# Performance work log

Hardware: AMD Instinct MI355X
Metric: run time of the kernel (lower is better)

Reference implementation:

```python
import jax, jax.numpy as jnp
import numpy as np

B, T, N, D = 16, 12, 325, 1
K, H = 3, 64
ST, Z, LH = 95, 32, 128
MI = ST + Z  # 127


def _mlp(x, w1, b1, w2, b2):
    return jnp.maximum(x @ w1 + b1, 0.0) @ w2 + b2


def setup_inputs() -> dict:
    key = jax.random.key(0)
    ks = jax.random.split(key, 20)
    inp = {
        "G": jax.random.normal(ks[0], (K, N, N), jnp.float32) * (1.0 / np.sqrt(N)),
        "x": jax.random.normal(ks[1], (B, T, N, D), jnp.float32),
        "meta_input": jax.random.normal(ks[2], (B, N, MI), jnp.float32),
    }
    s = 0.02
    outs = {"lwg": K * (D + H) * 2 * H, "lbg": 2 * H, "lwu": K * (D + H) * H, "lbu": H}
    i = 3
    for name, od in outs.items():
        inp[name + "_w1"] = jax.random.normal(ks[i], (MI, LH), jnp.float32) * s; i += 1
        inp[name + "_b1"] = jnp.zeros((LH,), jnp.float32)
        inp[name + "_w2"] = jax.random.normal(ks[i], (LH, od), jnp.float32) * s; i += 1
        inp[name + "_b2"] = jnp.zeros((od,), jnp.float32)
    return inp


def reference(G, x, meta_input,
              lwg_w1, lwg_b1, lwg_w2, lwg_b2,
              lbg_w1, lbg_b1, lbg_w2, lbg_b2,
              lwu_w1, lwu_b1, lwu_w2, lwu_b2,
              lbu_w1, lbu_b1, lbu_w2, lbu_b2):
    # hypernetwork: per-(batch, node) GCN weights
    Wg = _mlp(meta_input, lwg_w1, lwg_b1, lwg_w2, lwg_b2).reshape(B, N, K * (D + H), 2 * H)
    bg = _mlp(meta_input, lbg_w1, lbg_b1, lbg_w2, lbg_b2)          # [B,N,2H]
    Wu = _mlp(meta_input, lwu_w1, lwu_b1, lwu_w2, lwu_b2).reshape(B, N, K * (D + H), H)
    bu = _mlp(meta_input, lbu_w1, lbu_b1, lbu_w2, lbu_b2)          # [B,N,H]

    def gcn(inp, W, b):
        # Chebyshev hops stacked along k (matches torch.cat over k-blocks)
        sup = jnp.einsum('knm,bmi->bnki', G, inp)                  # [B,N,K,i]
        sup = sup.reshape(B, N, -1)                                # [B,N,K*i]
        return jnp.einsum('bni,bnih->bnh', sup, W) + b

    def step(h, xt):
        comb = jnp.concatenate([xt, h], axis=-1)                   # [B,N,D+H]
        zr = jax.nn.sigmoid(gcn(comb, Wg, bg))
        z, r = zr[..., :H], zr[..., H:]
        cand = jnp.concatenate([xt, r * h], axis=-1)
        n = jnp.tanh(gcn(cand, Wu, bu))
        h = z * n + (1.0 - z) * h
        return h, h

    h0 = jnp.zeros((B, N, H), x.dtype)
    h_last, hs = jax.lax.scan(step, h0, jnp.moveaxis(x, 1, 0))     # hs: [T,B,N,H]
    return jnp.moveaxis(hs, 0, 1), h_last
```

## Files before the change

kernel.cpp:

```cpp
#include <hip/hip_runtime.h>
#include <hip/hip_bf16.h>
#include <stdint.h>

#define Bc   16
#define Tc   12
#define Nc   325
#define Kc   3
#define Hc   64
#define MIc  127
#define LHc  128
#define BNc  (Bc*Nc)
#define SUPW 195
#define NCg  (SUPW*2*Hc)
#define NCu  (SUPW*Hc)
#define NT4  82
#define MP   163

typedef _Float16 half8  __attribute__((ext_vector_type(8)));
typedef _Float16 half2v __attribute__((ext_vector_type(2)));
typedef float    f32x4  __attribute__((ext_vector_type(4)));

static __device__ __forceinline__ float bflo(unsigned int u) {
    return __uint_as_float(u << 16);
}
static __device__ __forceinline__ float bfhi(unsigned int u) {
    return __uint_as_float(u & 0xffff0000u);
}
static __device__ __forceinline__ unsigned short f2bf(float f) {
    unsigned int u = __float_as_uint(f);
    unsigned int r = (u + 0x7fffu + ((u >> 16) & 1u)) >> 16;
    return (unsigned short)r;
}
static __device__ __forceinline__ float fdot2f(half2v a, half2v b, float c) {
#if defined(__has_builtin)
#if __has_builtin(__builtin_amdgcn_fdot2)
    return __builtin_amdgcn_fdot2(a, b, c, false);
#else
    return c + (float)a[0] * (float)b[0] + (float)a[1] * (float)b[1];
#endif
#else
    return c + (float)a[0] * (float)b[0] + (float)a[1] * (float)b[1];
#endif
}
static __device__ __forceinline__ unsigned int packh2(float a, float b) {
    half2v h; h[0] = (_Float16)a; h[1] = (_Float16)b;
    return *(unsigned int*)&h;
}

__global__ __launch_bounds__(128) void meta1_kernel(
    const float* __restrict__ meta,
    const float* __restrict__ w1a, const float* __restrict__ b1a,
    const float* __restrict__ w1b, const float* __restrict__ b1b,
    const float* __restrict__ w1c, const float* __restrict__ b1c,
    const float* __restrict__ w1d, const float* __restrict__ b1d,
    _Float16* __restrict__ r1a, _Float16* __restrict__ r1b,
    _Float16* __restrict__ r1c, _Float16* __restrict__ r1d)
{
    __shared__ float mrow[4][128];
    const int bn0 = blockIdx.x * 4;
    const int l   = threadIdx.x;
#pragma unroll
    for (int r = 0; r < 4; r++)
        mrow[r][l] = (l < MIc) ? meta[(size_t)(bn0 + r) * MIc + l] : 0.f;
    __syncthreads();

    const float* w1s[4] = {w1a, w1b, w1c, w1d};
    const float* b1s[4] = {b1a, b1b, b1c, b1d};
    _Float16*    os[4]  = {r1a, r1b, r1c, r1d};
#pragma unroll
    for (int s = 0; s < 4; s++) {
        const float* w = w1s[s];
        float acc[4];
        const float bv = b1s[s][l];
#pragma unroll
        for (int r = 0; r < 4; r++) acc[r] = bv;
        for (int m = 0; m < MIc; m++) {
            float wv = w[m * LHc + l];
#pragma unroll
            for (int r = 0; r < 4; r++) acc[r] = fmaf(mrow[r][m], wv, acc[r]);
        }
#pragma unroll
        for (int r = 0; r < 4; r++)
            os[s][(size_t)(bn0 + r) * LHc + l] = (_Float16)fmaxf(acc[r], 0.f);
    }
}

__global__ __launch_bounds__(256) void transpose_w2_kernel(
    const float* __restrict__ w2, _Float16* __restrict__ w2t, int NC)
{
    __shared__ float Ls[128][65];
    const int c0 = blockIdx.x * 64;
    const int t  = threadIdx.x;
    {
        const int c  = t & 63;
        const int kb = t >> 6;
        for (int k = kb; k < 128; k += 4) {
            int cc = c0 + c;
            Ls[k][c] = (cc < NC) ? w2[(size_t)k * NC + cc] : 0.f;
        }
    }
    __syncthreads();
    {
        const int k  = t & 127;
        const int ch = t >> 7;
        for (int c = ch; c < 64; c += 2) {
            int cc = c0 + c;
            if (cc < NC) w2t[(size_t)cc * 128 + k] = (_Float16)Ls[k][c];
        }
    }
}

template<bool BF16OUT>
__global__ __launch_bounds__(256) void meta2_mfma_kernel(
    const _Float16* __restrict__ A,
    const _Float16* __restrict__ Bt,
    const float* __restrict__ bias,
    void* __restrict__ outp, int NC, int nrows)
{
    __shared__ __align__(16) _Float16 As[64][136];
    __shared__ __align__(16) _Float16 Bs[64][136];
    __shared__ unsigned short Cs[64][72];
    const int t  = threadIdx.x;
    const int w  = t >> 6;
    const int l  = t & 63;
    const int r0 = blockIdx.x * 64;
    const int c0 = blockIdx.y * 64;

#pragma unroll
    for (int p = 0; p < 4; p++) {
        const int gid = p * 256 + t;
        const int row = gid >> 4;
        const int cg  = gid & 15;
        half8 av = (half8)(_Float16)0.f;
        if (r0 + row < nrows) av = *(const half8*)(A + (size_t)(r0 + row) * 128 + cg * 8);
        *(half8*)&As[row][cg * 8] = av;
        half8 bv = *(const half8*)(Bt + (size_t)(c0 + row) * 128 + cg * 8);
        *(half8*)&Bs[row][cg * 8] = bv;
    }
    __syncthreads();

    const int lr = l & 15;
    const int lk = l >> 4;

    half8 aF[4];
#pragma unroll
    for (int kk = 0; kk < 4; kk++)
        aF[kk] = *(const half8*)&As[w * 16 + lr][kk * 32 + lk * 8];

    f32x4 acc[4];
#pragma unroll
    for (int j = 0; j < 4; j++) acc[j] = (f32x4)0.f;

#pragma unroll
    for (int j = 0; j < 4; j++)
#pragma unroll
        for (int kk = 0; kk < 4; kk++) {
            half8 bF = *(const half8*)&Bs[j * 16 + lr][kk * 32 + lk * 8];
            acc[j] = __builtin_amdgcn_mfma_f32_16x16x32_f16(aF[kk], bF, acc[j], 0, 0, 0);
        }

    if (BF16OUT) {
#pragma unroll
        for (int j = 0; j < 4; j++) {
            const float bv = bias[c0 + j * 16 + lr];
#pragma unroll
            for (int q = 0; q < 4; q++)
                Cs[w * 16 + lk * 4 + q][j * 16 + lr] = f2bf(acc[j][q] + bv);
        }
        __syncthreads();
        const int rl  = t >> 2;
        const int cp  = t & 3;
        const int row = r0 + rl;
        if (row < nrows) {
            const uint4* src = (const uint4*)&Cs[rl][cp * 16];
            uint4* dst = (uint4*)((unsigned short*)outp + (size_t)row * NC + c0 + cp * 16);
            dst[0] = src[0];
            dst[1] = src[1];
        }
    } else {
#pragma unroll
        for (int j = 0; j < 4; j++) {
            const int col = c0 + j * 16 + lr;
            const float bv = bias[col];
#pragma unroll
            for (int q = 0; q < 4; q++) {
                const int row = r0 + w * 16 + lk * 4 + q;
                if (row < nrows)
                    ((float*)outp)[(size_t)row * NC + col] = acc[j][q] + bv;
            }
        }
    }
}

__global__ __launch_bounds__(256) void gx_kernel(
    const float* __restrict__ G, const float* __restrict__ x,
    float* __restrict__ GX)
{
    __shared__ __align__(16) float Gs[32][36];
    __shared__ __align__(16) float Xs[32][65];
    const int k   = blockIdx.x;
    const int n0  = blockIdx.y * 32;
    const int tb0 = blockIdx.z * 64;
    const int t   = threadIdx.x;
    const int j   = t & 63;
    const int ng  = t >> 6;

    float acc[8] = {0.f,0.f,0.f,0.f,0.f,0.f,0.f,0.f};

    for (int mc = 0; mc < 11; mc++) {
        const int m0 = mc * 32;
        __syncthreads();
        {
            const int ln  = t >> 3;
            const int lm0 = (t & 7) * 4;
            const int gn  = n0 + ln;
#pragma unroll
            for (int u = 0; u < 4; u++) {
                int m = m0 + lm0 + u;
                Gs[lm0 + u][ln] = (gn < Nc && m < Nc) ? G[((size_t)k * Nc + gn) * Nc + m] : 0.f;
            }
        }
        {
            const int row = t >> 2;
            const int ms  = (t & 3) * 8;
            const float* xr = x + (size_t)(tb0 + row) * Nc;
#pragma unroll
            for (int u = 0; u < 8; u++) {
                int m = m0 + ms + u;
                Xs[ms + u][row] = (m < Nc) ? xr[m] : 0.f;
            }
        }
        __syncthreads();
#pragma unroll
        for (int mm = 0; mm < 32; mm++) {
            float xv = Xs[mm][j];
            float4 ga = *(const float4*)&Gs[mm][ng * 8];
            float4 gb = *(const float4*)&Gs[mm][ng * 8 + 4];
            acc[0] = fmaf(ga.x, xv, acc[0]);
            acc[1] = fmaf(ga.y, xv, acc[1]);
            acc[2] = fmaf(ga.z, xv, acc[2]);
            acc[3] = fmaf(ga.w, xv, acc[3]);
            acc[4] = fmaf(gb.x, xv, acc[4]);
            acc[5] = fmaf(gb.y, xv, acc[5]);
            acc[6] = fmaf(gb.z, xv, acc[6]);
            acc[7] = fmaf(gb.w, xv, acc[7]);
        }
    }

    const int tb = tb0 + j;
    const int b  = tb / Tc;
    const int tv = tb % Tc;
    float* gxp = GX + (((size_t)tv * Bc + b) * Kc + k) * Nc;
#pragma unroll
    for (int i = 0; i < 8; i++) {
        int n = n0 + ng * 8 + i;
        if (n < Nc) gxp[n] = acc[i];
    }
}

__global__ __launch_bounds__(256) void fused_gates_kernel(
    const float* __restrict__ G, const float* __restrict__ hbuf,
    const float* __restrict__ GX, const unsigned short* __restrict__ Wg,
    const float* __restrict__ bg, float* __restrict__ zbuf,
    float* __restrict__ rhbuf, int tt, int bStart)
{
    __shared__ unsigned int Ht2[MP][64];
    __shared__ unsigned int Gt2[12][MP+1];
    __shared__ float supL[4][200];
    const int bx = blockIdx.x;
    const int bl = bx / NT4;
    const int n0 = (bx % NT4) * 4;
    const int b  = bStart + bl;
    const int t  = threadIdx.x;
    const int j  = t & 63;
    const int ng = t >> 6;

    {
        const float* hb = hbuf + (size_t)b * Nc * Hc;
        for (int mp = ng; mp < MP; mp += 4) {
            const int m0 = 2 * mp;
            float h0 = hb[(size_t)m0 * Hc + j];
            float h1 = (m0 + 1 < Nc) ? hb[(size_t)(m0 + 1) * Hc + j] : 0.f;
            Ht2[mp][j] = packh2(h0, h1);
        }
    }
#pragma unroll
    for (int r = 0; r < 12; r++) {
        const int nn = r / 3, k = r % 3;
        int n = n0 + nn; if (n >= Nc) n = Nc - 1;
        const float* gr = G + ((size_t)k * Nc + n) * Nc;
        for (int mp = t; mp < MP; mp += 256) {
            const int m0 = 2 * mp;
            float g0 = gr[m0];
            float g1 = (m0 + 1 < Nc) ? gr[m0 + 1] : 0.f;
            Gt2[r][mp] = packh2(g0, g1);
        }
    }
    __syncthreads();

    float a0 = 0.f, a1 = 0.f, a2v = 0.f;
    const unsigned int* g0p = &Gt2[ng * 3 + 0][0];
    const unsigned int* g1p = &Gt2[ng * 3 + 1][0];
    const unsigned int* g2p = &Gt2[ng * 3 + 2][0];
#pragma unroll 2
    for (int mp = 0; mp < MP; mp++) {
        unsigned int hu = Ht2[mp][j];
        half2v hh = *(half2v*)&hu;
        unsigned int u0 = g0p[mp], u1 = g1p[mp], u2 = g2p[mp];
        a0  = fdot2f(*(half2v*)&u0, hh, a0);
        a1  = fdot2f(*(half2v*)&u1, hh, a1);
        a2v = fdot2f(*(half2v*)&u2, hh, a2v);
    }
    supL[ng][0 * 65 + 1 + j] = a0;
    supL[ng][1 * 65 + 1 + j] = a1;
    supL[ng][2 * 65 + 1 + j] = a2v;
    if (t < 12) {
        const int nn = t / 3, k = t - (t / 3) * 3;
        const int n = n0 + nn;
        supL[nn][k * 65] = (n < Nc) ?
            GX[(((size_t)tt * Bc + b) * Kc + k) * Nc + n] : 0.f;
    }
    __syncthreads();

    const int n = n0 + ng;
    if (n >= Nc) return;
    const int lane = t & 63;
    const int c = lane & 15;
    const int g = lane >> 4;
    const size_t bnL = (size_t)bl * Nc + n;
    const size_t bng = (size_t)b  * Nc + n;
    const unsigned short* wrow = Wg + bnL * NCg;
    float a2[8] = {0.f,0.f,0.f,0.f,0.f,0.f,0.f,0.f};

    for (int i0 = 0; i0 < SUPW; i0 += 16) {
#pragma unroll
        for (int uu = 0; uu < 4; uu++) {
            const int i = i0 + uu * 4 + g;
            if (i < SUPW) {
                uint4 v = *(const uint4*)(wrow + (size_t)i * 128 + c * 8);
                float s = supL[ng][i];
                a2[0] = fmaf(s, bflo(v.x), a2[0]);
                a2[1] = fmaf(s, bfhi(v.x), a2[1]);
                a2[2] = fmaf(s, bflo(v.y), a2[2]);
                a2[3] = fmaf(s, bfhi(v.y), a2[3]);
                a2[4] = fmaf(s, bflo(v.z), a2[4]);
                a2[5] = fmaf(s, bfhi(v.z), a2[5]);
                a2[6] = fmaf(s, bflo(v.w), a2[6]);
                a2[7] = fmaf(s, bfhi(v.w), a2[7]);
            }
        }
    }
#pragma unroll
    for (int w8 = 0; w8 < 8; w8++) {
        a2[w8] += __shfl_xor(a2[w8], 16, 64);
        a2[w8] += __shfl_xor(a2[w8], 32, 64);
    }
    if (g == 0) {
#pragma unroll
        for (int w8 = 0; w8 < 8; w8++) {
            const int h2 = c * 8 + w8;
            const float pre = a2[w8] + bg[bng * (2 * Hc) + h2];
            const float zr  = 1.f / (1.f + expf(-pre));
            if (h2 < Hc) zbuf[bng * Hc + h2] = zr;
            else {
                const int hh = h2 - Hc;
                rhbuf[bng * Hc + hh] = zr * hbuf[bng * Hc + hh];
            }
        }
    }
}

__global__ __launch_bounds__(256) void fused_update_kernel(
    const float* __restrict__ G, const float* __restrict__ rhbuf,
    const float* __restrict__ GX, const unsigned short* __restrict__ Wu,
    const float* __restrict__ bu, const float* __restrict__ zbuf,
    float* __restrict__ hbuf, float* __restrict__ outp, int tt, int bStart)
{
    __shared__ unsigned int Ht2[MP][64];
    __shared__ unsigned int Gt2[12][MP+1];
    __shared__ float supL[4][200];
    const int bx = blockIdx.x;
    const int bl = bx / NT4;
    const int n0 = (bx % NT4) * 4;
    const int b  = bStart + bl;
    const int t  = threadIdx.x;
    const int j  = t & 63;
    const int ng = t >> 6;

    {
        const float* hb = rhbuf + (size_t)b * Nc * Hc;
        for (int mp = ng; mp < MP; mp += 4) {
            const int m0 = 2 * mp;
            float h0 = hb[(size_t)m0 * Hc + j];
            float h1 = (m0 + 1 < Nc) ? hb[(size_t)(m0 + 1) * Hc + j] : 0.f;
            Ht2[mp][j] = packh2(h0, h1);
        }
    }
#pragma unroll
    for (int r = 0; r < 12; r++) {
        const int nn = r / 3, k = r % 3;
        int n = n0 + nn; if (n >= Nc) n = Nc - 1;
        const float* gr = G + ((size_t)k * Nc + n) * Nc;
        for (int mp = t; mp < MP; mp += 256) {
            const int m0 = 2 * mp;
            float g0 = gr[m0];
            float g1 = (m0 + 1 < Nc) ? gr[m0 + 1] : 0.f;
            Gt2[r][mp] = packh2(g0, g1);
        }
    }
    __syncthreads();

    float a0 = 0.f, a1 = 0.f, a2v = 0.f;
    const unsigned int* g0p = &Gt2[ng * 3 + 0][0];
    const unsigned int* g1p = &Gt2[ng * 3 + 1][0];
    const unsigned int* g2p = &Gt2[ng * 3 + 2][0];
#pragma unroll 2
    for (int mp = 0; mp < MP; mp++) {
        unsigned int hu = Ht2[mp][j];
        half2v hh = *(half2v*)&hu;
        unsigned int u0 = g0p[mp], u1 = g1p[mp], u2 = g2p[mp];
        a0  = fdot2f(*(half2v*)&u0, hh, a0);
        a1  = fdot2f(*(half2v*)&u1, hh, a1);
        a2v = fdot2f(*(half2v*)&u2, hh, a2v);
    }
    supL[ng][0 * 65 + 1 + j] = a0;
    supL[ng][1 * 65 + 1 + j] = a1;
    supL[ng][2 * 65 + 1 + j] = a2v;
    if (t < 12) {
        const int nn = t / 3, k = t - (t / 3) * 3;
        const int n = n0 + nn;
        supL[nn][k * 65] = (n < Nc) ?
            GX[(((size_t)tt * Bc + b) * Kc + k) * Nc + n] : 0.f;
    }
    __syncthreads();

    const int n = n0 + ng;
    if (n >= Nc) return;
    const int lane = t & 63;
    const int c = lane & 7;
    const int g = lane >> 3;
    const size_t bnL = (size_t)bl * Nc + n;
    const size_t bng = (size_t)b  * Nc + n;
    const unsigned short* wrow = Wu + bnL * NCu;
    float a2[8] = {0.f,0.f,0.f,0.f,0.f,0.f,0.f,0.f};

    for (int i0 = 0; i0 < SUPW; i0 += 32) {
#pragma unroll
        for (int uu = 0; uu < 4; uu++) {
            const int i = i0 + uu * 8 + g;
            if (i < SUPW) {
                uint4 v = *(const uint4*)(wrow + (size_t)i * 64 + c * 8);
                float s = supL[ng][i];
                a2[0] = fmaf(s, bflo(v.x), a2[0]);
                a2[1] = fmaf(s, bfhi(v.x), a2[1]);
                a2[2] = fmaf(s, bflo(v.y), a2[2]);
                a2[3] = fmaf(s, bfhi(v.y), a2[3]);
                a2[4] = fmaf(s, bflo(v.z), a2[4]);
                a2[5] = fmaf(s, bfhi(v.z), a2[5]);
                a2[6] = fmaf(s, bflo(v.w), a2[6]);
                a2[7] = fmaf(s, bfhi(v.w), a2[7]);
            }
        }
    }
#pragma unroll
    for (int w8 = 0; w8 < 8; w8++) {
        a2[w8] += __shfl_xor(a2[w8], 8, 64);
        a2[w8] += __shfl_xor(a2[w8], 16, 64);
        a2[w8] += __shfl_xor(a2[w8], 32, 64);
    }
    if (g == 0) {
#pragma unroll
        for (int w8 = 0; w8 < 8; w8++) {
            const int hh = c * 8 + w8;
            const float npre = a2[w8] + bu[bng * Hc + hh];
            const float nn_t = tanhf(npre);
            const float z    = zbuf[bng * Hc + hh];
            const float hold = hbuf[bng * Hc + hh];
            const float hnew = fmaf(z, nn_t - hold, hold);
            hbuf[bng * Hc + hh] = hnew;
            outp[(((size_t)b * Tc + tt) * Nc + n) * Hc + hh] = hnew;
            if (tt == Tc - 1)
                outp[(size_t)Bc * Tc * Nc * Hc + bng * Hc + hh] = hnew;
        }
    }
}

extern "C" void kernel_launch(void* const* d_in, const int* in_sizes, int n_in,
                              void* d_out, int out_size, void* d_ws, size_t ws_size,
                              hipStream_t stream)
{
    const float* G        = (const float*)d_in[0];
    const float* x        = (const float*)d_in[1];
    const float* meta     = (const float*)d_in[2];
    const float* lwg_w1   = (const float*)d_in[3];
    const float* lwg_b1   = (const float*)d_in[4];
    const float* lwg_w2   = (const float*)d_in[5];
    const float* lwg_b2   = (const float*)d_in[6];
    const float* lbg_w1   = (const float*)d_in[7];
    const float* lbg_b1   = (const float*)d_in[8];
    const float* lbg_w2   = (const float*)d_in[9];
    const float* lbg_b2   = (const float*)d_in[10];
    const float* lwu_w1   = (const float*)d_in[11];
    const float* lwu_b1   = (const float*)d_in[12];
    const float* lwu_w2   = (const float*)d_in[13];
    const float* lwu_b2   = (const float*)d_in[14];
    const float* lbu_w1   = (const float*)d_in[15];
    const float* lbu_b1   = (const float*)d_in[16];
    const float* lbu_w2   = (const float*)d_in[17];
    const float* lbu_b2   = (const float*)d_in[18];

    auto alignup = [](size_t b) { return (b + 255) & ~(size_t)255; };
    const size_t miscBytes =
        alignup((size_t)BNc * 2 * Hc * 4) +
        alignup((size_t)BNc * Hc * 4) +
        4 * alignup((size_t)BNc * LHc * 2) +
        alignup((size_t)NCg * 128 * 2) +
        alignup((size_t)NCu * 128 * 2) +
        alignup((size_t)128 * 128 * 2) +
        alignup((size_t)64 * 128 * 2) +
        alignup((size_t)Tc * Bc * Kc * Nc * 4) +
        3 * alignup((size_t)BNc * Hc * 4);

    int Bch = 0;
    const int cand[4] = {8, 4, 2, 1};
    for (int ci = 0; ci < 4; ci++) {
        size_t BNch = (size_t)cand[ci] * Nc;
        size_t need = miscBytes + alignup(BNch * NCg * 2) + alignup(BNch * NCu * 2);
        if (need <= ws_size) { Bch = cand[ci]; break; }
    }
    if (Bch == 0) return;
    const int nChunks = Bc / Bch;
    const int BNch    = Bch * Nc;

    char* ws = (char*)d_ws;
    size_t off = 0;
    auto alloc = [&](size_t bytes) -> char* {
        char* p = ws + off;
        off += (bytes + 255) & ~(size_t)255;
        return p;
    };
    unsigned short* Wg = (unsigned short*)alloc((size_t)BNch * NCg * 2);
    unsigned short* Wu = (unsigned short*)alloc((size_t)BNch * NCu * 2);
    float* bgbuf  = (float*)alloc((size_t)BNc * 2 * Hc * 4);
    float* bubuf  = (float*)alloc((size_t)BNc * Hc * 4);
    _Float16* r1g  = (_Float16*)alloc((size_t)BNc * LHc * 2);
    _Float16* r1bg = (_Float16*)alloc((size_t)BNc * LHc * 2);
    _Float16* r1u  = (_Float16*)alloc((size_t)BNc * LHc * 2);
    _Float16* r1bu = (_Float16*)alloc((size_t)BNc * LHc * 2);
    _Float16* w2tg  = (_Float16*)alloc((size_t)NCg * 128 * 2);
    _Float16* w2tu  = (_Float16*)alloc((size_t)NCu * 128 * 2);
    _Float16* w2tbg = (_Float16*)alloc((size_t)128 * 128 * 2);
    _Float16* w2tbu = (_Float16*)alloc((size_t)64 * 128 * 2);
    float* GX    = (float*)alloc((size_t)Tc * Bc * Kc * Nc * 4);
    float* hbuf  = (float*)alloc((size_t)BNc * Hc * 4);
    float* zbuf  = (float*)alloc((size_t)BNc * Hc * 4);
    float* rhbuf = (float*)alloc((size_t)BNc * Hc * 4);
    if (off > ws_size) return;

    float* out = (float*)d_out;

    hipMemsetAsync(hbuf, 0, (size_t)BNc * Hc * 4, stream);

    meta1_kernel<<<BNc / 4, 128, 0, stream>>>(
        meta, lwg_w1, lwg_b1, lbg_w1, lbg_b1, lwu_w1, lwu_b1, lbu_w1, lbu_b1,
        r1g, r1bg, r1u, r1bu);

    transpose_w2_kernel<<<(NCg + 63) / 64, 256, 0, stream>>>(lwg_w2, w2tg, NCg);
    transpose_w2_kernel<<<(NCu + 63) / 64, 256, 0, stream>>>(lwu_w2, w2tu, NCu);
    transpose_w2_kernel<<<2, 256, 0, stream>>>(lbg_w2, w2tbg, 2 * Hc);
    transpose_w2_kernel<<<1, 256, 0, stream>>>(lbu_w2, w2tbu, Hc);

    meta2_mfma_kernel<false><<<dim3((BNc + 63) / 64, (2 * Hc) / 64), 256, 0, stream>>>(
        r1bg, w2tbg, lbg_b2, (void*)bgbuf, 2 * Hc, BNc);
    meta2_mfma_kernel<false><<<dim3((BNc + 63) / 64, Hc / 64), 256, 0, stream>>>(
        r1bu, w2tbu, lbu_b2, (void*)bubuf, Hc, BNc);

    gx_kernel<<<dim3(Kc, 11, 3), 256, 0, stream>>>(G, x, GX);

    for (int ch = 0; ch < nChunks; ch++) {
        const int bStart  = ch * Bch;
        const int bnStart = bStart * Nc;

        meta2_mfma_kernel<true><<<dim3((BNch + 63) / 64, NCg / 64), 256, 0, stream>>>(
            r1g + (size_t)bnStart * LHc, w2tg, lwg_b2, (void*)Wg, NCg, BNch);
        meta2_mfma_kernel<true><<<dim3((BNch + 63) / 64, NCu / 64), 256, 0, stream>>>(
            r1u + (size_t)bnStart * LHc, w2tu, lwu_b2, (void*)Wu, NCu, BNch);

        for (int tt = 0; tt < Tc; tt++) {
            fused_gates_kernel<<<Bch * NT4, 256, 0, stream>>>(
                G, hbuf, GX, Wg, bgbuf, zbuf, rhbuf, tt, bStart);
            fused_update_kernel<<<Bch * NT4, 256, 0, stream>>>(
                G, rhbuf, GX, Wu, bubuf, zbuf, hbuf, out, tt, bStart);
        }
    }
}
```

Before: 2.369 ms.

## Assign one node per block and chunk graph-diffusion staging through small LDS tiles

Fused gate and update kernels now process a single node per block, staging the hidden state and G rows in 32-pair chunks rather than whole-matrix LDS buffers. The weight GEMV is split across all four waves, with partial sums reduced through shared memory. LDS use shrinks sharply and the launch bound requests six blocks per CU to raise occupancy. In exchange, each block re-reads and repacks the full hidden state for only one node, which quadruples that traffic and adds per-chunk barriers.

```diff
diff --git a/kernel.cpp b/kernel.cpp
--- a/kernel.cpp
+++ b/kernel.cpp
@@ -13,8 +13,8 @@
 #define SUPW 195
 #define NCg  (SUPW*2*Hc)
 #define NCu  (SUPW*Hc)
-#define NT4  82
 #define MP   163
+#define MCH  6
 
 typedef _Float16 half8  __attribute__((ext_vector_type(8)));
 typedef _Float16 half2v __attribute__((ext_vector_type(2)));
@@ -258,108 +258,104 @@
     }
 }
 
-__global__ __launch_bounds__(256) void fused_gates_kernel(
+__global__ __launch_bounds__(256, 6) void fused_gates_kernel(
     const float* __restrict__ G, const float* __restrict__ hbuf,
     const float* __restrict__ GX, const unsigned short* __restrict__ Wg,
     const float* __restrict__ bg, float* __restrict__ zbuf,
     float* __restrict__ rhbuf, int tt, int bStart)
 {
-    __shared__ unsigned int Ht2[MP][64];
-    __shared__ unsigned int Gt2[12][MP+1];
-    __shared__ float supL[4][200];
+    __shared__ unsigned int Hc2[32][64];
+    __shared__ unsigned int Gc2[3][34];
+    __shared__ float supL[208];
+    __shared__ float pS[4][16][8];
     const int bx = blockIdx.x;
-    const int bl = bx / NT4;
-    const int n0 = (bx % NT4) * 4;
+    const int bl = bx / Nc;
+    const int n  = bx % Nc;
     const int b  = bStart + bl;
     const int t  = threadIdx.x;
-    const int j  = t & 63;
-    const int ng = t >> 6;
-
-    {
-        const float* hb = hbuf + (size_t)b * Nc * Hc;
-        for (int mp = ng; mp < MP; mp += 4) {
-            const int m0 = 2 * mp;
-            float h0 = hb[(size_t)m0 * Hc + j];
-            float h1 = (m0 + 1 < Nc) ? hb[(size_t)(m0 + 1) * Hc + j] : 0.f;
-            Ht2[mp][j] = packh2(h0, h1);
-        }
-    }
-#pragma unroll
-    for (int r = 0; r < 12; r++) {
-        const int nn = r / 3, k = r % 3;
-        int n = n0 + nn; if (n >= Nc) n = Nc - 1;
-        const float* gr = G + ((size_t)k * Nc + n) * Nc;
-        for (int mp = t; mp < MP; mp += 256) {
-            const int m0 = 2 * mp;
-            float g0 = gr[m0];
+    const int lane = t & 63;
+    const int w  = t >> 6;
+    const int j  = lane;
+
+    const float* hb = hbuf + (size_t)b * Nc * Hc;
+    float accA = 0.f;
+
+    for (int c6 = 0; c6 < MCH; c6++) {
+        const int mpB = c6 * 32;
+        __syncthreads();
+#pragma unroll
+        for (int p = 0; p < 8; p++) {
+            const int idx = p * 256 + t;
+            const int mpl = idx >> 6;
+            const int jj  = idx & 63;
+            const int m0  = 2 * (mpB + mpl);
+            float h0 = (m0 < Nc)     ? hb[(size_t)m0 * Hc + jj]       : 0.f;
+            float h1 = (m0 + 1 < Nc) ? hb[(size_t)(m0 + 1) * Hc + jj] : 0.f;
+            Hc2[mpl][jj] = packh2(h0, h1);
+        }
+        if (t < 96) {
+            const int kk  = t >> 5;
+            const int mpl = t & 31;
+            const int m0  = 2 * (mpB + mpl);
+            const float* gr = G + ((size_t)kk * Nc + n) * Nc;
+            float g0 = (m0 < Nc)     ? gr[m0]     : 0.f;
             float g1 = (m0 + 1 < Nc) ? gr[m0 + 1] : 0.f;
-            Gt2[r][mp] = packh2(g0, g1);
-        }
-    }
-    __syncthreads();
-
-    float a0 = 0.f, a1 = 0.f, a2v = 0.f;
-    const unsigned int* g0p = &Gt2[ng * 3 + 0][0];
-    const unsigned int* g1p = &Gt2[ng * 3 + 1][0];
-    const unsigned int* g2p = &Gt2[ng * 3 + 2][0];
-#pragma unroll 2
-    for (int mp = 0; mp < MP; mp++) {
-        unsigned int hu = Ht2[mp][j];
-        half2v hh = *(half2v*)&hu;
-        unsigned int u0 = g0p[mp], u1 = g1p[mp], u2 = g2p[mp];
-        a0  = fdot2f(*(half2v*)&u0, hh, a0);
-        a1  = fdot2f(*(half2v*)&u1, hh, a1);
-        a2v = fdot2f(*(half2v*)&u2, hh, a2v);
-    }
-    supL[ng][0 * 65 + 1 + j] = a0;
-    supL[ng][1 * 65 + 1 + j] = a1;
-    supL[ng][2 * 65 + 1 + j] = a2v;
-    if (t < 12) {
-        const int nn = t / 3, k = t - (t / 3) * 3;
-        const int n = n0 + nn;
-        supL[nn][k * 65] = (n < Nc) ?
-            GX[(((size_t)tt * Bc + b) * Kc + k) * Nc + n] : 0.f;
-    }
-    __syncthreads();
-
-    const int n = n0 + ng;
-    if (n >= Nc) return;
-    const int lane = t & 63;
+            Gc2[kk][mpl] = packh2(g0, g1);
+        }
+        __syncthreads();
+        if (w < 3) {
+            const unsigned int* gp = &Gc2[w][0];
+#pragma unroll
+            for (int mpl = 0; mpl < 32; mpl++) {
+                unsigned int hu = Hc2[mpl][j];
+                unsigned int gu = gp[mpl];
+                accA = fdot2f(*(half2v*)&gu, *(half2v*)&hu, accA);
+            }
+        }
+    }
+    if (w < 3) supL[w * 65 + 1 + j] = accA;
+    if (t < 3)
+        supL[t * 65] = GX[(((size_t)tt * Bc + b) * Kc + t) * Nc + n];
+    __syncthreads();
+
     const int c = lane & 15;
     const int g = lane >> 4;
-    const size_t bnL = (size_t)bl * Nc + n;
-    const size_t bng = (size_t)b  * Nc + n;
-    const unsigned short* wrow = Wg + bnL * NCg;
+    const unsigned short* wrow = Wg + ((size_t)bl * Nc + n) * NCg;
     float a2[8] = {0.f,0.f,0.f,0.f,0.f,0.f,0.f,0.f};
 
+#pragma unroll
     for (int i0 = 0; i0 < SUPW; i0 += 16) {
-#pragma unroll
-        for (int uu = 0; uu < 4; uu++) {
-            const int i = i0 + uu * 4 + g;
-            if (i < SUPW) {
-                uint4 v = *(const uint4*)(wrow + (size_t)i * 128 + c * 8);
-                float s = supL[ng][i];
-                a2[0] = fmaf(s, bflo(v.x), a2[0]);
-                a2[1] = fmaf(s, bfhi(v.x), a2[1]);
-                a2[2] = fmaf(s, bflo(v.y), a2[2]);
-                a2[3] = fmaf(s, bfhi(v.y), a2[3]);
-                a2[4] = fmaf(s, bflo(v.z), a2[4]);
-                a2[5] = fmaf(s, bfhi(v.z), a2[5]);
-                a2[6] = fmaf(s, bflo(v.w), a2[6]);
-                a2[7] = fmaf(s, bfhi(v.w), a2[7]);
-            }
-        }
-    }
-#pragma unroll
-    for (int w8 = 0; w8 < 8; w8++) {
-        a2[w8] += __shfl_xor(a2[w8], 16, 64);
-        a2[w8] += __shfl_xor(a2[w8], 32, 64);
+        const int i = i0 + w * 4 + g;
+        if (i < SUPW) {
+            uint4 v = *(const uint4*)(wrow + (size_t)i * 128 + c * 8);
+            float s = supL[i];
+            a2[0] = fmaf(s, bflo(v.x), a2[0]);
+            a2[1] = fmaf(s, bfhi(v.x), a2[1]);
+            a2[2] = fmaf(s, bflo(v.y), a2[2]);
+            a2[3] = fmaf(s, bfhi(v.y), a2[3]);
+            a2[4] = fmaf(s, bflo(v.z), a2[4]);
+            a2[5] = fmaf(s, bfhi(v.z), a2[5]);
+            a2[6] = fmaf(s, bflo(v.w), a2[6]);
+            a2[7] = fmaf(s, bfhi(v.w), a2[7]);
+        }
+    }
+#pragma unroll
+    for (int e = 0; e < 8; e++) {
+        a2[e] += __shfl_xor(a2[e], 16, 64);
+        a2[e] += __shfl_xor(a2[e], 32, 64);
     }
     if (g == 0) {
 #pragma unroll
-        for (int w8 = 0; w8 < 8; w8++) {
-            const int h2 = c * 8 + w8;
-            const float pre = a2[w8] + bg[bng * (2 * Hc) + h2];
+        for (int e = 0; e < 8; e++) pS[w][c][e] = a2[e];
+    }
+    __syncthreads();
+    if (w == 0 && g == 0) {
+        const size_t bng = (size_t)b * Nc + n;
+#pragma unroll
+        for (int e = 0; e < 8; e++) {
+            const int h2 = c * 8 + e;
+            const float pre = pS[0][c][e] + pS[1][c][e] + pS[2][c][e] + pS[3][c][e]
+                            + bg[bng * (2 * Hc) + h2];
             const float zr  = 1.f / (1.f + expf(-pre));
             if (h2 < Hc) zbuf[bng * Hc + h2] = zr;
             else {
@@ -370,109 +366,105 @@
     }
 }
 
-__global__ __launch_bounds__(256) void fused_update_kernel(
+__global__ __launch_bounds__(256, 6) void fused_update_kernel(
     const float* __restrict__ G, const float* __restrict__ rhbuf,
     const float* __restrict__ GX, const unsigned short* __restrict__ Wu,
     const float* __restrict__ bu, const float* __restrict__ zbuf,
     float* __restrict__ hbuf, float* __restrict__ outp, int tt, int bStart)
 {
-    __shared__ unsigned int Ht2[MP][64];
-    __shared__ unsigned int Gt2[12][MP+1];
-    __shared__ float supL[4][200];
+    __shared__ unsigned int Hc2[32][64];
+    __shared__ unsigned int Gc2[3][34];
+    __shared__ float supL[208];
+    __shared__ float pS[4][8][8];
     const int bx = blockIdx.x;
-    const int bl = bx / NT4;
-    const int n0 = (bx % NT4) * 4;
+    const int bl = bx / Nc;
+    const int n  = bx % Nc;
     const int b  = bStart + bl;
     const int t  = threadIdx.x;
-    const int j  = t & 63;
-    const int ng = t >> 6;
-
-    {
-        const float* hb = rhbuf + (size_t)b * Nc * Hc;
-        for (int mp = ng; mp < MP; mp += 4) {
-            const int m0 = 2 * mp;
-            float h0 = hb[(size_t)m0 * Hc + j];
-            float h1 = (m0 + 1 < Nc) ? hb[(size_t)(m0 + 1) * Hc + j] : 0.f;
-            Ht2[mp][j] = packh2(h0, h1);
-        }
-    }
-#pragma unroll
-    for (int r = 0; r < 12; r++) {
-        const int nn = r / 3, k = r % 3;
-        int n = n0 + nn; if (n >= Nc) n = Nc - 1;
-        const float* gr = G + ((size_t)k * Nc + n) * Nc;
-        for (int mp = t; mp < MP; mp += 256) {
-            const int m0 = 2 * mp;
-            float g0 = gr[m0];
+    const int lane = t & 63;
+    const int w  = t >> 6;
+    const int j  = lane;
+
+    const float* hb = rhbuf + (size_t)b * Nc * Hc;
+    float accA = 0.f;
+
+    for (int c6 = 0; c6 < MCH; c6++) {
+        const int mpB = c6 * 32;
+        __syncthreads();
+#pragma unroll
+        for (int p = 0; p < 8; p++) {
+            const int idx = p * 256 + t;
+            const int mpl = idx >> 6;
+            const int jj  = idx & 63;
+            const int m0  = 2 * (mpB + mpl);
+            float h0 = (m0 < Nc)     ? hb[(size_t)m0 * Hc + jj]       : 0.f;
+            float h1 = (m0 + 1 < Nc) ? hb[(size_t)(m0 + 1) * Hc + jj] : 0.f;
+            Hc2[mpl][jj] = packh2(h0, h1);
+        }
+        if (t < 96) {
+            const int kk  = t >> 5;
+            const int mpl = t & 31;
+            const int m0  = 2 * (mpB + mpl);
+            const float* gr = G + ((size_t)kk * Nc + n) * Nc;
+            float g0 = (m0 < Nc)     ? gr[m0]     : 0.f;
             float g1 = (m0 + 1 < Nc) ? gr[m0 + 1] : 0.f;
-            Gt2[r][mp] = packh2(g0, g1);
-        }
-    }
-    __syncthreads();
-
-    float a0 = 0.f, a1 = 0.f, a2v = 0.f;
-    const unsigned int* g0p = &Gt2[ng * 3 + 0][0];
-    const unsigned int* g1p = &Gt2[ng * 3 + 1][0];
-    const unsigned int* g2p = &Gt2[ng * 3 + 2][0];
-#pragma unroll 2
-    for (int mp = 0; mp < MP; mp++) {
-        unsigned int hu = Ht2[mp][j];
-        half2v hh = *(half2v*)&hu;
-        unsigned int u0 = g0p[mp], u1 = g1p[mp], u2 = g2p[mp];
-        a0  = fdot2f(*(half2v*)&u0, hh, a0);
-        a1  = fdot2f(*(half2v*)&u1, hh, a1);
-        a2v = fdot2f(*(half2v*)&u2, hh, a2v);
-    }
-    supL[ng][0 * 65 + 1 + j] = a0;
-    supL[ng][1 * 65 + 1 + j] = a1;
-    supL[ng][2 * 65 + 1 + j] = a2v;
-    if (t < 12) {
-        const int nn = t / 3, k = t - (t / 3) * 3;
-        const int n = n0 + nn;
-        supL[nn][k * 65] = (n < Nc) ?
-            GX[(((size_t)tt * Bc + b) * Kc + k) * Nc + n] : 0.f;
-    }
-    __syncthreads();
-
-    const int n = n0 + ng;
-    if (n >= Nc) return;
-    const int lane = t & 63;
+            Gc2[kk][mpl] = packh2(g0, g1);
+        }
+        __syncthreads();
+        if (w < 3) {
+            const unsigned int* gp = &Gc2[w][0];
+#pragma unroll
+            for (int mpl = 0; mpl < 32; mpl++) {
+                unsigned int hu = Hc2[mpl][j];
+                unsigned int gu = gp[mpl];
+                accA = fdot2f(*(half2v*)&gu, *(half2v*)&hu, accA);
+            }
+        }
+    }
+    if (w < 3) supL[w * 65 + 1 + j] = accA;
+    if (t < 3)
+        supL[t * 65] = GX[(((size_t)tt * Bc + b) * Kc + t) * Nc + n];
+    __syncthreads();
+
     const int c = lane & 7;
     const int g = lane >> 3;
-    const size_t bnL = (size_t)bl * Nc + n;
-    const size_t bng = (size_t)b  * Nc + n;
-    const unsigned short* wrow = Wu + bnL * NCu;
+    const unsigned short* wrow = Wu + ((size_t)bl * Nc + n) * NCu;
     float a2[8] = {0.f,0.f,0.f,0.f,0.f,0.f,0.f,0.f};
 
+#pragma unroll
     for (int i0 = 0; i0 < SUPW; i0 += 32) {
-#pragma unroll
-        for (int uu = 0; uu < 4; uu++) {
-            const int i = i0 + uu * 8 + g;
-            if (i < SUPW) {
-                uint4 v = *(const uint4*)(wrow + (size_t)i * 64 + c * 8);
-                float s = supL[ng][i];
-                a2[0] = fmaf(s, bflo(v.x), a2[0]);
-                a2[1] = fmaf(s, bfhi(v.x), a2[1]);
-                a2[2] = fmaf(s, bflo(v.y), a2[2]);
-                a2[3] = fmaf(s, bfhi(v.y), a2[3]);
-                a2[4] = fmaf(s, bflo(v.z), a2[4]);
-                a2[5] = fmaf(s, bfhi(v.z), a2[5]);
-                a2[6] = fmaf(s, bflo(v.w), a2[6]);
-                a2[7] = fmaf(s, bfhi(v.w), a2[7]);
-            }
-        }
-    }
-#pragma unroll
-    for (int w8 = 0; w8 < 8; w8++) {
-        a2[w8] += __shfl_xor(a2[w8], 8, 64);
-        a2[w8] += __shfl_xor(a2[w8], 16, 64);
-        a2[w8] += __shfl_xor(a2[w8], 32, 64);
+        const int i = i0 + w * 8 + g;
+        if (i < SUPW) {
+            uint4 v = *(const uint4*)(wrow + (size_t)i * 64 + c * 8);
+            float s = supL[i];
+            a2[0] = fmaf(s, bflo(v.x), a2[0]);
+            a2[1] = fmaf(s, bfhi(v.x), a2[1]);
+            a2[2] = fmaf(s, bflo(v.y), a2[2]);
+            a2[3] = fmaf(s, bfhi(v.y), a2[3]);
+            a2[4] = fmaf(s, bflo(v.z), a2[4]);
+            a2[5] = fmaf(s, bfhi(v.z), a2[5]);
+            a2[6] = fmaf(s, bflo(v.w), a2[6]);
+            a2[7] = fmaf(s, bfhi(v.w), a2[7]);
+        }
+    }
+#pragma unroll
+    for (int e = 0; e < 8; e++) {
+        a2[e] += __shfl_xor(a2[e], 8, 64);
+        a2[e] += __shfl_xor(a2[e], 16, 64);
+        a2[e] += __shfl_xor(a2[e], 32, 64);
     }
     if (g == 0) {
 #pragma unroll
-        for (int w8 = 0; w8 < 8; w8++) {
-            const int hh = c * 8 + w8;
-            const float npre = a2[w8] + bu[bng * Hc + hh];
+        for (int e = 0; e < 8; e++) pS[w][c][e] = a2[e];
+    }
+    __syncthreads();
+    if (w == 0 && g == 0) {
+        const size_t bng = (size_t)b * Nc + n;
+#pragma unroll
+        for (int e = 0; e < 8; e++) {
+            const int hh = c * 8 + e;
+            const float npre = pS[0][c][e] + pS[1][c][e] + pS[2][c][e] + pS[3][c][e]
+                             + bu[bng * Hc + hh];
             const float nn_t = tanhf(npre);
             const float z    = zbuf[bng * Hc + hh];
             const float hold = hbuf[bng * Hc + hh];
@@ -587,9 +579,9 @@
             r1u + (size_t)bnStart * LHc, w2tu, lwu_b2, (void*)Wu, NCu, BNch);
 
         for (int tt = 0; tt < Tc; tt++) {
-            fused_gates_kernel<<<Bch * NT4, 256, 0, stream>>>(
+            fused_gates_kernel<<<Bch * Nc, 256, 0, stream>>>(
                 G, hbuf, GX, Wg, bgbuf, zbuf, rhbuf, tt, bStart);
-            fused_update_kernel<<<Bch * NT4, 256, 0, stream>>>(
+            fused_update_kernel<<<Bch * Nc, 256, 0, stream>>>(
                 G, rhbuf, GX, Wu, bubuf, zbuf, hbuf, out, tt, bStart);
         }
     }
```

New measurement: 2.141 ms. 1.11x faster.
